# Kernel optimization log

Hardware: AMD Instinct MI355X
Metric: run time of the kernel (lower is better)

Reference implementation:

```python
import jax, jax.numpy as jnp
import numpy as np

VOCAB = 50257
EMB = 512
HID = 1024
H = HID // 2  # per-direction hidden
TAGS = 24
START = 22
STOP = 23
SEQ = 4096
NEG = -10000.0


def setup_inputs() -> dict:
    key = jax.random.key(0)
    ks = jax.random.split(key, 16)
    s = 1.0 / np.sqrt(H)
    u = lambda k, shp: jax.random.uniform(k, shp, jnp.float32, -s, s)
    sentence = jax.random.randint(ks[0], (SEQ,), 0, VOCAB)
    emb = jax.random.normal(ks[1], (VOCAB, EMB), jnp.float32)
    w_ih_f = u(ks[2], (4 * H, EMB)); w_hh_f = u(ks[3], (4 * H, H))
    b_ih_f = u(ks[4], (4 * H,));    b_hh_f = u(ks[5], (4 * H,))
    w_ih_b = u(ks[6], (4 * H, EMB)); w_hh_b = u(ks[7], (4 * H, H))
    b_ih_b = u(ks[8], (4 * H,));    b_hh_b = u(ks[9], (4 * H,))
    w_tag = u(ks[10], (TAGS, HID)); b_tag = u(ks[11], (TAGS,))
    transitions = jax.random.normal(ks[12], (TAGS, TAGS), jnp.float32)
    transitions = transitions.at[START, :].set(NEG).at[:, STOP].set(NEG)
    h0 = jax.random.normal(ks[13], (2, H), jnp.float32)  # [dir, H]
    c0 = jax.random.normal(ks[14], (2, H), jnp.float32)
    return dict(sentence=sentence, emb=emb,
                w_ih_f=w_ih_f, w_hh_f=w_hh_f, b_ih_f=b_ih_f, b_hh_f=b_hh_f,
                w_ih_b=w_ih_b, w_hh_b=w_hh_b, b_ih_b=b_ih_b, b_hh_b=b_hh_b,
                w_tag=w_tag, b_tag=b_tag, transitions=transitions, h0=h0, c0=c0)


def _lstm_dir(x, w_ih, w_hh, b_ih, b_hh, h, c, reverse):
    # x: [T, EMB]; precompute input projections once
    xg = x @ w_ih.T + (b_ih + b_hh)  # [T, 4H]
    def step(carry, xt):
        h, c = carry
        g = xt + h @ w_hh.T
        i, f, gg, o = jnp.split(g, 4)
        i = jax.nn.sigmoid(i); f = jax.nn.sigmoid(f)
        gg = jnp.tanh(gg);     o = jax.nn.sigmoid(o)
        c = f * c + i * gg
        h = o * jnp.tanh(c)
        return (h, c), h
    _, hs = jax.lax.scan(step, (h, c), xg, reverse=reverse)
    return hs  # [T, H]


def reference(sentence, emb, w_ih_f, w_hh_f, b_ih_f, b_hh_f,
              w_ih_b, w_hh_b, b_ih_b, b_hh_b, w_tag, b_tag,
              transitions, h0, c0):
    x = emb[sentence]  # [T, EMB]
    hf = _lstm_dir(x, w_ih_f, w_hh_f, b_ih_f, b_hh_f, h0[0], c0[0], False)
    hb = _lstm_dir(x, w_ih_b, w_hh_b, b_ih_b, b_hh_b, h0[1], c0[1], True)
    lstm_out = jnp.concatenate([hf, hb], axis=-1)          # [T, HID]
    feats = lstm_out @ w_tag.T + b_tag                     # [T, TAGS]

    # Viterbi: max-plus recursion over tags, vectorized per timestep
    fv0 = jnp.full((TAGS,), NEG, jnp.float32).at[START].set(0.0)
    def vstep(fv, feat):
        scores = transitions + fv[None, :]                 # [next, prev]
        bp = jnp.argmax(scores, axis=1)
        return jnp.max(scores, axis=1) + feat, bp
    fv, bps = jax.lax.scan(vstep, fv0, feats)              # bps: [T, TAGS]

    terminal = fv + transitions[STOP]
    best = jnp.argmax(terminal)
    path_score = terminal[best]

    def btstep(tag, bp):
        prev = bp[tag]
        return prev, prev
    _, ys = jax.lax.scan(btstep, best, bps, reverse=True)  # ys[t] = tag at t-1; ys[0]==START
    best_path = jnp.concatenate([ys[1:], best[None]]).astype(jnp.int32)
    return path_score, best_path
```

## Files before the change

### kernel.cpp

```cpp
#include <hip/hip_runtime.h>
#include <cstdint>
#include <cstddef>

#define T_SEQ 4096
#define EMB_D 512
#define HDIM 512
#define G4 2048
#define NTAGS 24
#define START_TAG 22
#define STOP_TAG 23
#define NEGV -10000.0f
#define NBLK 32
#define HSLICE 16
#define SENT 0xFFFFFFFFu

__global__ __launch_bounds__(256) void gemm_xg_kernel(
    const int* __restrict__ sent, const float* __restrict__ emb,
    const float* __restrict__ w_ih_f, const float* __restrict__ b_ih_f, const float* __restrict__ b_hh_f,
    const float* __restrict__ w_ih_b, const float* __restrict__ b_ih_b, const float* __restrict__ b_hh_b,
    float* __restrict__ xg)
{
    const int dir = blockIdx.z;
    const float* W  = dir ? w_ih_b : w_ih_f;
    const float* bi = dir ? b_ih_b : b_ih_f;
    const float* bh = dir ? b_hh_b : b_hh_f;
    const int m0 = blockIdx.y * 64;
    const int n0 = blockIdx.x * 64;
    const int tid = threadIdx.x;

    __shared__ __attribute__((aligned(16))) float As[32][64];
    __shared__ __attribute__((aligned(16))) float Bs[32][64];

    const int lrow = tid >> 2;
    const int lk   = (tid & 3) * 8;

    const int srow = sent[m0 + lrow];
    const float* aptr = emb + (size_t)srow * EMB_D + lk;
    const float* bptr = W   + (size_t)(n0 + lrow) * EMB_D + lk;

    const int ty = tid >> 4;
    const int tx = tid & 15;

    float acc[4][4];
    #pragma unroll
    for (int i = 0; i < 4; ++i)
        #pragma unroll
        for (int j = 0; j < 4; ++j) acc[i][j] = 0.f;

    for (int kk = 0; kk < EMB_D; kk += 32) {
        float4 a0 = *(const float4*)(aptr + kk);
        float4 a1 = *(const float4*)(aptr + kk + 4);
        float4 b0 = *(const float4*)(bptr + kk);
        float4 b1 = *(const float4*)(bptr + kk + 4);
        __syncthreads();
        As[lk+0][lrow]=a0.x; As[lk+1][lrow]=a0.y; As[lk+2][lrow]=a0.z; As[lk+3][lrow]=a0.w;
        As[lk+4][lrow]=a1.x; As[lk+5][lrow]=a1.y; As[lk+6][lrow]=a1.z; As[lk+7][lrow]=a1.w;
        Bs[lk+0][lrow]=b0.x; Bs[lk+1][lrow]=b0.y; Bs[lk+2][lrow]=b0.z; Bs[lk+3][lrow]=b0.w;
        Bs[lk+4][lrow]=b1.x; Bs[lk+5][lrow]=b1.y; Bs[lk+6][lrow]=b1.z; Bs[lk+7][lrow]=b1.w;
        __syncthreads();
        #pragma unroll
        for (int k = 0; k < 32; ++k) {
            float4 av = *(const float4*)&As[k][ty*4];
            float4 bv = *(const float4*)&Bs[k][tx*4];
            acc[0][0]+=av.x*bv.x; acc[0][1]+=av.x*bv.y; acc[0][2]+=av.x*bv.z; acc[0][3]+=av.x*bv.w;
            acc[1][0]+=av.y*bv.x; acc[1][1]+=av.y*bv.y; acc[1][2]+=av.y*bv.z; acc[1][3]+=av.y*bv.w;
            acc[2][0]+=av.z*bv.x; acc[2][1]+=av.z*bv.y; acc[2][2]+=av.z*bv.z; acc[2][3]+=av.z*bv.w;
            acc[3][0]+=av.w*bv.x; acc[3][1]+=av.w*bv.y; acc[3][2]+=av.w*bv.z; acc[3][3]+=av.w*bv.w;
        }
    }
    #pragma unroll
    for (int i = 0; i < 4; ++i) {
        const int t = m0 + ty*4 + i;
        float* crow = xg + ((size_t)dir*T_SEQ + t) * G4 + n0 + tx*4;
        #pragma unroll
        for (int j = 0; j < 4; ++j) {
            const int jg = n0 + tx*4 + j;
            crow[j] = acc[i][j] + bi[jg] + bh[jg];
        }
    }
}

__global__ __attribute__((amdgpu_waves_per_eu(2, 2))) __launch_bounds__(512)
void bilstm_kernel(
    const float* __restrict__ w_hh_f, const float* __restrict__ w_hh_b,
    const float* __restrict__ h0, const float* __restrict__ c0,
    const float* __restrict__ xg,
    uint32_t* __restrict__ h_hist,
    int* __restrict__ claim)
{
    uint32_t xcc;
    asm volatile("s_getreg_b32 %0, hwreg(HW_REG_XCC_ID)" : "=s"(xcc));
    xcc &= 7u;

    __shared__ int rank_s;
    if (threadIdx.x == 0)
        rank_s = __hip_atomic_fetch_add(&claim[xcc], 1, __ATOMIC_RELAXED,
                                        __HIP_MEMORY_SCOPE_AGENT);
    __syncthreads();
    const int rank = rank_s;

    int dir;
    if (xcc == 0) dir = 0;
    else if (xcc == 1) dir = 1;
    else return;
    if (rank >= NBLK) return;
    const int b = rank;

    const int tid = threadIdx.x;
    const int q   = tid >> 6;
    const int l   = tid & 63;
    const int r   = l >> 3;
    const int i   = l & 7;
    const int gate = r & 3;
    const int huo  = r >> 2;
    const int row  = gate * HDIM + b * HSLICE + 2*q + huo;

    const float* Wrow = (dir ? w_hh_b : w_hh_f) + (size_t)row * HDIM + i * 64;
    float w[64];
    #pragma unroll
    for (int j = 0; j < 16; ++j) {
        float4 v = ((const float4*)Wrow)[j];
        w[4*j+0]=v.x; w[4*j+1]=v.y; w[4*j+2]=v.z; w[4*j+3]=v.w;
    }
    #pragma unroll
    for (int ii = 0; ii < 64; ++ii) asm volatile("" : "+v"(w[ii]));

    __shared__ __attribute__((aligned(16))) float hbuf[2][544];

    float c = 0.f;
    if (i == 0 && gate == 0)
        c = c0[dir*HDIM + b*HSLICE + 2*q + huo];

    const float* xgd = xg + (size_t)dir * T_SEQ * G4;
    uint32_t* hh = h_hist + (size_t)dir * T_SEQ * HDIM;
    const bool leader = (i == 0);

    float xv_cur = 0.f;
    if (leader) {
        const int t0 = dir ? (T_SEQ - 1) : 0;
        xv_cur = xgd[(size_t)t0 * G4 + row];
    }

    for (int idx = 0; idx < T_SEQ; ++idx) {
        const int t = dir ? (T_SEQ - 1 - idx) : idx;
        const int p = idx & 1;

        float hv;
        if (idx == 0) {
            hv = h0[dir*HDIM + tid];
        } else {
            const int tprev = dir ? (t + 1) : (t - 1);
            const uint32_t* wp = hh + (size_t)tprev*HDIM + tid;
            uint32_t u;
            do {
                u = __hip_atomic_load(wp, __ATOMIC_RELAXED, __HIP_MEMORY_SCOPE_AGENT);
            } while (u == SENT);
            union { uint32_t uu; float f; } cv; cv.uu = u;
            hv = cv.f;
        }
        hbuf[p][q*68 + l] = hv;
        __syncthreads();

        float xv_nxt = 0.f;
        if (leader && idx + 1 < T_SEQ) {
            const int tn = dir ? (t - 1) : (t + 1);
            xv_nxt = xgd[(size_t)tn * G4 + row];
        }

        const float4* hb4 = (const float4*)&hbuf[p][i*68];
        float s = 0.f;
        #pragma unroll
        for (int j = 0; j < 16; ++j) {
            float4 hvv = hb4[j];
            s += w[4*j+0]*hvv.x + w[4*j+1]*hvv.y + w[4*j+2]*hvv.z + w[4*j+3]*hvv.w;
        }

        const int gbase = l & ~7;
        float g = xv_cur + s;
        #pragma unroll
        for (int j = 1; j < 8; ++j) {
            float pj = __shfl(s, gbase + j);
            g += pj;
        }

        float act = (gate == 2) ? tanhf(g) : 1.f/(1.f + expf(-g));

        const int base = l & 32;
        float iv = __shfl(act, base + 0);
        float fg = __shfl(act, base + 8);
        float gv = __shfl(act, base + 16);
        float ov = __shfl(act, base + 24);

        if ((l & 31) == 0) {
            c = fg*c + iv*gv;
            union { float f; uint32_t u; } hb; hb.f = ov * tanhf(c);
            __hip_atomic_store(hh + (size_t)t*HDIM + b*HSLICE + 2*q + (l>>5), hb.u,
                               __ATOMIC_RELAXED, __HIP_MEMORY_SCOPE_AGENT);
        }
        xv_cur = xv_nxt;
    }
}

__global__ __launch_bounds__(256) void feats_kernel(
    const float* __restrict__ h_hist, const float* __restrict__ w_tag,
    const float* __restrict__ b_tag, float* __restrict__ feats)
{
    const int t = blockIdx.x;
    const int tid = threadIdx.x;
    __shared__ __attribute__((aligned(16))) float h[1024];
    __shared__ float partl[192];
    for (int i = tid; i < 512; i += 256) {
        h[i]     = h_hist[(size_t)t*HDIM + i];
        h[512+i] = h_hist[(size_t)T_SEQ*HDIM + (size_t)t*HDIM + i];
    }
    __syncthreads();
    if (tid < 192) {
        const int tag = tid >> 3, p = tid & 7;
        const float* wr = w_tag + (size_t)tag*1024 + p*128;
        const float* hp = h + p*128;
        float s = 0.f;
        #pragma unroll 8
        for (int j = 0; j < 128; ++j) s += wr[j]*hp[j];
        partl[tid] = s;
    }
    __syncthreads();
    if (tid < NTAGS) {
        float s = b_tag[tid];
        #pragma unroll
        for (int p = 0; p < 8; ++p) s += partl[tid*8+p];
        feats[(size_t)t*NTAGS + tid] = s;
    }
}

__global__ void viterbi_fwd_kernel(
    const float* __restrict__ feats, const float* __restrict__ trans,
    float* __restrict__ d_out, unsigned char* __restrict__ bp,
    int* __restrict__ best_tag)
{
    const int lane = threadIdx.x;
    const bool act = lane < NTAGS;
    float tr[NTAGS];
    #pragma unroll
    for (int p = 0; p < NTAGS; ++p)
        tr[p] = act ? trans[lane*NTAGS + p] : NEGV;

    float fv = (lane == START_TAG) ? 0.f : NEGV;
    __shared__ float fvs[NTAGS];
    __shared__ float term[NTAGS];

    float ftn = act ? feats[lane] : 0.f;
    for (int t = 0; t < T_SEQ; ++t) {
        if (act) fvs[lane] = fv;
        __syncthreads();
        float ft = ftn;
        if (act && t + 1 < T_SEQ) ftn = feats[(size_t)(t+1)*NTAGS + lane];
        float bestv = -3.4e38f;
        int argp = 0;
        #pragma unroll
        for (int p = 0; p < NTAGS; ++p) {
            float sc = tr[p] + fvs[p];
            if (sc > bestv) { bestv = sc; argp = p; }
        }
        __syncthreads();
        fv = bestv + ft;
        if (act) bp[(size_t)t*NTAGS + lane] = (unsigned char)argp;
    }
    if (act) { fv += trans[STOP_TAG*NTAGS + lane]; term[lane] = fv; }
    __syncthreads();
    if (lane == 0) {
        float bv = term[0]; int bi = 0;
        #pragma unroll
        for (int p = 1; p < NTAGS; ++p) if (term[p] > bv) { bv = term[p]; bi = p; }
        d_out[0] = bv;
        *best_tag = bi;
    }
}

__global__ void bt_compose_kernel(const unsigned char* __restrict__ bp,
                                  unsigned char* __restrict__ segmap)
{
    const int s = blockIdx.x;
    const int tid = threadIdx.x;
    __shared__ __attribute__((aligned(16))) unsigned char lbp[64*NTAGS];
    const uint32_t* src = (const uint32_t*)(bp + (size_t)s * 64 * NTAGS);
    uint32_t* dst = (uint32_t*)lbp;
    #pragma unroll
    for (int i = 0; i < 6; ++i) dst[tid + 64*i] = src[tid + 64*i];
    __syncthreads();
    if (tid < NTAGS) {
        int m = tid;
        for (int tt = 63; tt >= 0; --tt) m = lbp[tt*NTAGS + m];
        segmap[s*NTAGS + tid] = (unsigned char)m;
    }
}

__global__ void bt_final_kernel(const unsigned char* __restrict__ segmap,
                                const int* __restrict__ best_tag,
                                int* __restrict__ end_tags)
{
    if (threadIdx.x == 0) {
        int tag = *best_tag;
        end_tags[63] = tag;
        for (int s = 63; s >= 1; --s) {
            tag = segmap[s*NTAGS + tag];
            end_tags[s-1] = tag;
        }
    }
}

__global__ void bt_write_kernel(const unsigned char* __restrict__ bp,
                                const int* __restrict__ end_tags,
                                float* __restrict__ out_path)
{
    const int s = blockIdx.x;
    const int tid = threadIdx.x;
    __shared__ __attribute__((aligned(16))) unsigned char lbp[64*NTAGS];
    const uint32_t* src = (const uint32_t*)(bp + (size_t)s * 64 * NTAGS);
    uint32_t* dst = (uint32_t*)lbp;
    #pragma unroll
    for (int i = 0; i < 6; ++i) dst[tid + 64*i] = src[tid + 64*i];
    __syncthreads();
    if (tid == 0) {
        int tag = end_tags[s];
        out_path[s*64 + 63] = (float)tag;
        for (int tt = 63; tt >= 1; --tt) {
            tag = lbp[tt*NTAGS + tag];
            out_path[s*64 + tt - 1] = (float)tag;
        }
    }
}

extern "C" void kernel_launch(void* const* d_in, const int* in_sizes, int n_in,
                              void* d_out, int out_size, void* d_ws, size_t ws_size,
                              hipStream_t stream)
{
    const int*   sent   = (const int*)d_in[0];
    const float* emb    = (const float*)d_in[1];
    const float* w_ih_f = (const float*)d_in[2];
    const float* w_hh_f = (const float*)d_in[3];
    const float* b_ih_f = (const float*)d_in[4];
    const float* b_hh_f = (const float*)d_in[5];
    const float* w_ih_b = (const float*)d_in[6];
    const float* w_hh_b = (const float*)d_in[7];
    const float* b_ih_b = (const float*)d_in[8];
    const float* b_hh_b = (const float*)d_in[9];
    const float* w_tag  = (const float*)d_in[10];
    const float* b_tag  = (const float*)d_in[11];
    const float* trans  = (const float*)d_in[12];
    const float* h0     = (const float*)d_in[13];
    const float* c0     = (const float*)d_in[14];
    float* out = (float*)d_out;

    char* ws = (char*)d_ws;
    size_t off = 0;
    auto alloc = [&](size_t bytes) {
        char* p = ws + off; off += (bytes + 255) & ~(size_t)255; return p;
    };
    float* xg      = (float*)alloc((size_t)2*T_SEQ*G4*sizeof(float));
    uint32_t* h_hist = (uint32_t*)alloc((size_t)2*T_SEQ*HDIM*sizeof(float));
    float* feats   = (float*)alloc((size_t)T_SEQ*NTAGS*sizeof(float));
    unsigned char* bp     = (unsigned char*)alloc((size_t)T_SEQ*NTAGS);
    unsigned char* segmap = (unsigned char*)alloc(64*NTAGS);
    int* best_tag = (int*)alloc(sizeof(int));
    int* end_tags = (int*)alloc(64*sizeof(int));
    int* claim    = (int*)alloc(8*sizeof(int));

    if (off > ws_size) {
        hipMemsetAsync(d_out, 0xFF, 4, stream);
        return;
    }

    hipMemsetAsync(h_hist, 0xFF, (size_t)2*T_SEQ*HDIM*sizeof(float), stream);
    hipMemsetAsync(claim, 0, 8*sizeof(int), stream);

    dim3 gg(G4/64, T_SEQ/64, 2);
    gemm_xg_kernel<<<gg, 256, 0, stream>>>(sent, emb,
        w_ih_f, b_ih_f, b_hh_f, w_ih_b, b_ih_b, b_hh_b, xg);
    bilstm_kernel<<<512, 512, 0, stream>>>(w_hh_f, w_hh_b, h0, c0, xg, h_hist, claim);
    feats_kernel<<<T_SEQ, 256, 0, stream>>>((const float*)h_hist, w_tag, b_tag, feats);
    viterbi_fwd_kernel<<<1, 64, 0, stream>>>(feats, trans, out, bp, best_tag);
    bt_compose_kernel<<<64, 64, 0, stream>>>(bp, segmap);
    bt_final_kernel<<<1, 64, 0, stream>>>(segmap, best_tag, end_tags);
    bt_write_kernel<<<64, 64, 0, stream>>>(bp, end_tags, out + 1);
}
```

Baseline: 8.296 ms.

## Fuse input-projection GEMM into persistent BiLSTM kernel with sentinel-based overlap

```diff
diff --git a/kernel.cpp b/kernel.cpp
--- a/kernel.cpp
+++ b/kernel.cpp
@@ -13,100 +13,101 @@
 #define NBLK 32
 #define HSLICE 16
 #define SENT 0xFFFFFFFFu
-
-__global__ __launch_bounds__(256) void gemm_xg_kernel(
+#define NTILES 4096
+
+__global__ __attribute__((amdgpu_waves_per_eu(2, 2))) __launch_bounds__(512)
+void fused_kernel(
     const int* __restrict__ sent, const float* __restrict__ emb,
     const float* __restrict__ w_ih_f, const float* __restrict__ b_ih_f, const float* __restrict__ b_hh_f,
     const float* __restrict__ w_ih_b, const float* __restrict__ b_ih_b, const float* __restrict__ b_hh_b,
-    float* __restrict__ xg)
-{
-    const int dir = blockIdx.z;
-    const float* W  = dir ? w_ih_b : w_ih_f;
-    const float* bi = dir ? b_ih_b : b_ih_f;
-    const float* bh = dir ? b_hh_b : b_hh_f;
-    const int m0 = blockIdx.y * 64;
-    const int n0 = blockIdx.x * 64;
-    const int tid = threadIdx.x;
-
-    __shared__ __attribute__((aligned(16))) float As[32][64];
-    __shared__ __attribute__((aligned(16))) float Bs[32][64];
-
-    const int lrow = tid >> 2;
-    const int lk   = (tid & 3) * 8;
-
-    const int srow = sent[m0 + lrow];
-    const float* aptr = emb + (size_t)srow * EMB_D + lk;
-    const float* bptr = W   + (size_t)(n0 + lrow) * EMB_D + lk;
-
-    const int ty = tid >> 4;
-    const int tx = tid & 15;
-
-    float acc[4][4];
-    #pragma unroll
-    for (int i = 0; i < 4; ++i)
-        #pragma unroll
-        for (int j = 0; j < 4; ++j) acc[i][j] = 0.f;
-
-    for (int kk = 0; kk < EMB_D; kk += 32) {
-        float4 a0 = *(const float4*)(aptr + kk);
-        float4 a1 = *(const float4*)(aptr + kk + 4);
-        float4 b0 = *(const float4*)(bptr + kk);
-        float4 b1 = *(const float4*)(bptr + kk + 4);
-        __syncthreads();
-        As[lk+0][lrow]=a0.x; As[lk+1][lrow]=a0.y; As[lk+2][lrow]=a0.z; As[lk+3][lrow]=a0.w;
-        As[lk+4][lrow]=a1.x; As[lk+5][lrow]=a1.y; As[lk+6][lrow]=a1.z; As[lk+7][lrow]=a1.w;
-        Bs[lk+0][lrow]=b0.x; Bs[lk+1][lrow]=b0.y; Bs[lk+2][lrow]=b0.z; Bs[lk+3][lrow]=b0.w;
-        Bs[lk+4][lrow]=b1.x; Bs[lk+5][lrow]=b1.y; Bs[lk+6][lrow]=b1.z; Bs[lk+7][lrow]=b1.w;
-        __syncthreads();
-        #pragma unroll
-        for (int k = 0; k < 32; ++k) {
-            float4 av = *(const float4*)&As[k][ty*4];
-            float4 bv = *(const float4*)&Bs[k][tx*4];
-            acc[0][0]+=av.x*bv.x; acc[0][1]+=av.x*bv.y; acc[0][2]+=av.x*bv.z; acc[0][3]+=av.x*bv.w;
-            acc[1][0]+=av.y*bv.x; acc[1][1]+=av.y*bv.y; acc[1][2]+=av.y*bv.z; acc[1][3]+=av.y*bv.w;
-            acc[2][0]+=av.z*bv.x; acc[2][1]+=av.z*bv.y; acc[2][2]+=av.z*bv.z; acc[2][3]+=av.z*bv.w;
-            acc[3][0]+=av.w*bv.x; acc[3][1]+=av.w*bv.y; acc[3][2]+=av.w*bv.z; acc[3][3]+=av.w*bv.w;
-        }
-    }
-    #pragma unroll
-    for (int i = 0; i < 4; ++i) {
-        const int t = m0 + ty*4 + i;
-        float* crow = xg + ((size_t)dir*T_SEQ + t) * G4 + n0 + tx*4;
-        #pragma unroll
-        for (int j = 0; j < 4; ++j) {
-            const int jg = n0 + tx*4 + j;
-            crow[j] = acc[i][j] + bi[jg] + bh[jg];
-        }
-    }
-}
-
-__global__ __attribute__((amdgpu_waves_per_eu(2, 2))) __launch_bounds__(512)
-void bilstm_kernel(
     const float* __restrict__ w_hh_f, const float* __restrict__ w_hh_b,
     const float* __restrict__ h0, const float* __restrict__ c0,
-    const float* __restrict__ xg,
+    uint32_t* __restrict__ xg,
     uint32_t* __restrict__ h_hist,
-    int* __restrict__ claim)
-{
+    int* __restrict__ claim,
+    int* __restrict__ tilectr)
+{
+    __shared__ __attribute__((aligned(16))) float smem[4096];
+    __shared__ int rank_s;
+    __shared__ int g_s;
+
     uint32_t xcc;
     asm volatile("s_getreg_b32 %0, hwreg(HW_REG_XCC_ID)" : "=s"(xcc));
     xcc &= 7u;
-
-    __shared__ int rank_s;
-    if (threadIdx.x == 0)
+    const int tid = threadIdx.x;
+
+    if (tid == 0)
         rank_s = __hip_atomic_fetch_add(&claim[xcc], 1, __ATOMIC_RELAXED,
                                         __HIP_MEMORY_SCOPE_AGENT);
     __syncthreads();
     const int rank = rank_s;
 
-    int dir;
-    if (xcc == 0) dir = 0;
-    else if (xcc == 1) dir = 1;
-    else return;
+    if (xcc >= 2) {
+        float* As = smem;
+        float* Bs = smem + 2048;
+        const int lrow = tid >> 3;
+        const int lk4  = (tid & 7) * 4;
+        const int ty = tid >> 5;
+        const int tx = tid & 31;
+        for (;;) {
+            if (tid == 0)
+                g_s = __hip_atomic_fetch_add(tilectr, 1, __ATOMIC_RELAXED,
+                                             __HIP_MEMORY_SCOPE_AGENT);
+            __syncthreads();
+            const int g = g_s;
+            if (g >= NTILES) break;
+            const int tt  = g >> 6;
+            const int dir = (g >> 5) & 1;
+            const int jt  = g & 31;
+            const int mt  = dir ? (63 - tt) : tt;
+            const int m0 = mt * 64, n0 = jt * 64;
+            const float* W  = dir ? w_ih_b : w_ih_f;
+            const float* bi = dir ? b_ih_b : b_ih_f;
+            const float* bh = dir ? b_hh_b : b_hh_f;
+            const int srow = sent[m0 + lrow];
+            const float* aptr = emb + (size_t)srow * EMB_D + lk4;
+            const float* bptr = W   + (size_t)(n0 + lrow) * EMB_D + lk4;
+            float acc[4][2];
+            #pragma unroll
+            for (int i2 = 0; i2 < 4; ++i2) { acc[i2][0] = 0.f; acc[i2][1] = 0.f; }
+            for (int kk = 0; kk < EMB_D; kk += 32) {
+                float4 a  = *(const float4*)(aptr + kk);
+                float4 bv = *(const float4*)(bptr + kk);
+                __syncthreads();
+                As[(lk4+0)*64+lrow]=a.x;  As[(lk4+1)*64+lrow]=a.y;
+                As[(lk4+2)*64+lrow]=a.z;  As[(lk4+3)*64+lrow]=a.w;
+                Bs[(lk4+0)*64+lrow]=bv.x; Bs[(lk4+1)*64+lrow]=bv.y;
+                Bs[(lk4+2)*64+lrow]=bv.z; Bs[(lk4+3)*64+lrow]=bv.w;
+                __syncthreads();
+                #pragma unroll
+                for (int k = 0; k < 32; ++k) {
+                    float4 av = *(const float4*)&As[k*64 + ty*4];
+                    float2 bb = *(const float2*)&Bs[k*64 + tx*2];
+                    acc[0][0]+=av.x*bb.x; acc[0][1]+=av.x*bb.y;
+                    acc[1][0]+=av.y*bb.x; acc[1][1]+=av.y*bb.y;
+                    acc[2][0]+=av.z*bb.x; acc[2][1]+=av.z*bb.y;
+                    acc[3][0]+=av.w*bb.x; acc[3][1]+=av.w*bb.y;
+                }
+            }
+            #pragma unroll
+            for (int i2 = 0; i2 < 4; ++i2) {
+                const int t = m0 + ty*4 + i2;
+                uint32_t* crow = xg + ((size_t)dir*T_SEQ + t) * G4 + n0 + tx*2;
+                const int jg = n0 + tx*2;
+                union { float f; uint32_t u; } v0, v1;
+                v0.f = acc[i2][0] + bi[jg]   + bh[jg];
+                v1.f = acc[i2][1] + bi[jg+1] + bh[jg+1];
+                __hip_atomic_store(crow + 0, v0.u, __ATOMIC_RELAXED, __HIP_MEMORY_SCOPE_AGENT);
+                __hip_atomic_store(crow + 1, v1.u, __ATOMIC_RELAXED, __HIP_MEMORY_SCOPE_AGENT);
+            }
+        }
+        return;
+    }
+
     if (rank >= NBLK) return;
+    const int dir = (int)xcc;
     const int b = rank;
 
-    const int tid = threadIdx.x;
     const int q   = tid >> 6;
     const int l   = tid & 63;
     const int r   = l >> 3;
@@ -125,25 +126,25 @@
     #pragma unroll
     for (int ii = 0; ii < 64; ++ii) asm volatile("" : "+v"(w[ii]));
 
-    __shared__ __attribute__((aligned(16))) float hbuf[2][544];
-
     float c = 0.f;
     if (i == 0 && gate == 0)
         c = c0[dir*HDIM + b*HSLICE + 2*q + huo];
 
-    const float* xgd = xg + (size_t)dir * T_SEQ * G4;
+    const uint32_t* xgu = xg + (size_t)dir * T_SEQ * G4;
     uint32_t* hh = h_hist + (size_t)dir * T_SEQ * HDIM;
     const bool leader = (i == 0);
 
-    float xv_cur = 0.f;
+    uint32_t xu_cur = 0;
+    const uint32_t* xp_cur = xgu;
     if (leader) {
         const int t0 = dir ? (T_SEQ - 1) : 0;
-        xv_cur = xgd[(size_t)t0 * G4 + row];
+        xp_cur = xgu + (size_t)t0 * G4 + row;
+        xu_cur = __hip_atomic_load(xp_cur, __ATOMIC_RELAXED, __HIP_MEMORY_SCOPE_AGENT);
     }
 
     for (int idx = 0; idx < T_SEQ; ++idx) {
         const int t = dir ? (T_SEQ - 1 - idx) : idx;
-        const int p = idx & 1;
+        float* hb = smem + (idx & 1) * 544;
 
         float hv;
         if (idx == 0) {
@@ -158,16 +159,22 @@
             union { uint32_t uu; float f; } cv; cv.uu = u;
             hv = cv.f;
         }
-        hbuf[p][q*68 + l] = hv;
+        hb[q*68 + l] = hv;
         __syncthreads();
 
-        float xv_nxt = 0.f;
+        float xv_cur = 0.f;
+        if (leader) {
+            while (xu_cur == SENT)
+                xu_cur = __hip_atomic_load(xp_cur, __ATOMIC_RELAXED, __HIP_MEMORY_SCOPE_AGENT);
+            xv_cur = __uint_as_float(xu_cur);
+        }
         if (leader && idx + 1 < T_SEQ) {
             const int tn = dir ? (t - 1) : (t + 1);
-            xv_nxt = xgd[(size_t)tn * G4 + row];
-        }
-
-        const float4* hb4 = (const float4*)&hbuf[p][i*68];
+            xp_cur = xgu + (size_t)tn * G4 + row;
+            xu_cur = __hip_atomic_load(xp_cur, __ATOMIC_RELAXED, __HIP_MEMORY_SCOPE_AGENT);
+        }
+
+        const float4* hb4 = (const float4*)&hb[i*68];
         float s = 0.f;
         #pragma unroll
         for (int j = 0; j < 16; ++j) {
@@ -193,11 +200,10 @@
 
         if ((l & 31) == 0) {
             c = fg*c + iv*gv;
-            union { float f; uint32_t u; } hb; hb.f = ov * tanhf(c);
-            __hip_atomic_store(hh + (size_t)t*HDIM + b*HSLICE + 2*q + (l>>5), hb.u,
+            union { float f; uint32_t u; } hbv; hbv.f = ov * tanhf(c);
+            __hip_atomic_store(hh + (size_t)t*HDIM + b*HSLICE + 2*q + (l>>5), hbv.u,
                                __ATOMIC_RELAXED, __HIP_MEMORY_SCOPE_AGENT);
         }
-        xv_cur = xv_nxt;
     }
 }
 
@@ -356,7 +362,7 @@
     auto alloc = [&](size_t bytes) {
         char* p = ws + off; off += (bytes + 255) & ~(size_t)255; return p;
     };
-    float* xg      = (float*)alloc((size_t)2*T_SEQ*G4*sizeof(float));
+    uint32_t* xg     = (uint32_t*)alloc((size_t)2*T_SEQ*G4*sizeof(float));
     uint32_t* h_hist = (uint32_t*)alloc((size_t)2*T_SEQ*HDIM*sizeof(float));
     float* feats   = (float*)alloc((size_t)T_SEQ*NTAGS*sizeof(float));
     unsigned char* bp     = (unsigned char*)alloc((size_t)T_SEQ*NTAGS);
@@ -364,19 +370,23 @@
     int* best_tag = (int*)alloc(sizeof(int));
     int* end_tags = (int*)alloc(64*sizeof(int));
     int* claim    = (int*)alloc(8*sizeof(int));
+    int* tilectr  = (int*)alloc(sizeof(int));
 
     if (off > ws_size) {
         hipMemsetAsync(d_out, 0xFF, 4, stream);
         return;
     }
 
+    hipMemsetAsync(xg,     0xFF, (size_t)2*T_SEQ*G4*sizeof(float), stream);
     hipMemsetAsync(h_hist, 0xFF, (size_t)2*T_SEQ*HDIM*sizeof(float), stream);
     hipMemsetAsync(claim, 0, 8*sizeof(int), stream);
-
-    dim3 gg(G4/64, T_SEQ/64, 2);
-    gemm_xg_kernel<<<gg, 256, 0, stream>>>(sent, emb,
-        w_ih_f, b_ih_f, b_hh_f, w_ih_b, b_ih_b, b_hh_b, xg);
-    bilstm_kernel<<<512, 512, 0, stream>>>(w_hh_f, w_hh_b, h0, c0, xg, h_hist, claim);
+    hipMemsetAsync(tilectr, 0, sizeof(int), stream);
+
+    fused_kernel<<<512, 512, 0, stream>>>(
+        sent, emb,
+        w_ih_f, b_ih_f, b_hh_f, w_ih_b, b_ih_b, b_hh_b,
+        w_hh_f, w_hh_b, h0, c0,
+        xg, h_hist, claim, tilectr);
     feats_kernel<<<T_SEQ, 256, 0, stream>>>((const float*)h_hist, w_tag, b_tag, feats);
     viterbi_fwd_kernel<<<1, 64, 0, stream>>>(feats, trans, out, bp, best_tag);
     bt_compose_kernel<<<64, 64, 0, stream>>>(bp, segmap);
```

Result: slower. 16.69 ms (+101.2%).

## Shorten Viterbi step latency: drop barriers, tree argmax, deeper feature prefetch

Applied to the files above, without the earlier changes.

```diff
diff --git a/kernel.cpp b/kernel.cpp
--- a/kernel.cpp
+++ b/kernel.cpp
@@ -245,28 +245,63 @@
         tr[p] = act ? trans[lane*NTAGS + p] : NEGV;
 
     float fv = (lane == START_TAG) ? 0.f : NEGV;
-    __shared__ float fvs[NTAGS];
+    __shared__ __attribute__((aligned(16))) float fvs[NTAGS];
     __shared__ float term[NTAGS];
 
-    float ftn = act ? feats[lane] : 0.f;
-    for (int t = 0; t < T_SEQ; ++t) {
-        if (act) fvs[lane] = fv;
-        __syncthreads();
-        float ft = ftn;
-        if (act && t + 1 < T_SEQ) ftn = feats[(size_t)(t+1)*NTAGS + lane];
-        float bestv = -3.4e38f;
-        int argp = 0;
-        #pragma unroll
-        for (int p = 0; p < NTAGS; ++p) {
-            float sc = tr[p] + fvs[p];
-            if (sc > bestv) { bestv = sc; argp = p; }
-        }
-        __syncthreads();
-        fv = bestv + ft;
-        if (act) bp[(size_t)t*NTAGS + lane] = (unsigned char)argp;
+    float fpre[8];
+    #pragma unroll
+    for (int k = 0; k < 8; ++k)
+        fpre[k] = act ? feats[(size_t)k*NTAGS + lane] : 0.f;
+
+    for (int t0 = 0; t0 < T_SEQ; t0 += 8) {
+        #pragma unroll
+        for (int k = 0; k < 8; ++k) {
+            const int t = t0 + k;
+            const float ft = fpre[k];
+            if (act && t + 8 < T_SEQ)
+                fpre[k] = feats[(size_t)(t + 8)*NTAGS + lane];
+
+            if (act) fvs[lane] = fv;
+            float fp[24];
+            #pragma unroll
+            for (int v = 0; v < 6; ++v)
+                *(float4*)&fp[v*4] = *(const float4*)&fvs[v*4];
+
+            float sc[24];
+            #pragma unroll
+            for (int p = 0; p < NTAGS; ++p) sc[p] = tr[p] + fp[p];
+
+            float v12[12]; int i12[12];
+            #pragma unroll
+            for (int p = 0; p < 12; ++p) {
+                const bool g2 = sc[2*p+1] > sc[2*p];
+                v12[p] = g2 ? sc[2*p+1] : sc[2*p];
+                i12[p] = g2 ? (2*p+1) : (2*p);
+            }
+            float v6[6]; int i6[6];
+            #pragma unroll
+            for (int p = 0; p < 6; ++p) {
+                const bool g2 = v12[2*p+1] > v12[2*p];
+                v6[p] = g2 ? v12[2*p+1] : v12[2*p];
+                i6[p] = g2 ? i12[2*p+1] : i12[2*p];
+            }
+            float v3[3]; int i3[3];
+            #pragma unroll
+            for (int p = 0; p < 3; ++p) {
+                const bool g2 = v6[2*p+1] > v6[2*p];
+                v3[p] = g2 ? v6[2*p+1] : v6[2*p];
+                i3[p] = g2 ? i6[2*p+1] : i6[2*p];
+            }
+            float bv01 = (v3[1] > v3[0]) ? v3[1] : v3[0];
+            int   bi01 = (v3[1] > v3[0]) ? i3[1] : i3[0];
+            const float bestv = (v3[2] > bv01) ? v3[2] : bv01;
+            const int   argp  = (v3[2] > bv01) ? i3[2] : bi01;
+
+            fv = bestv + ft;
+            if (act) bp[(size_t)t*NTAGS + lane] = (unsigned char)argp;
+        }
     }
     if (act) { fv += trans[STOP_TAG*NTAGS + lane]; term[lane] = fv; }
-    __syncthreads();
     if (lane == 0) {
         float bv = term[0]; int bi = 0;
         #pragma unroll
```

Measured after the change: 7.728 ms. 6.8% less time.
